# Performance work log

Measured on AMD Instinct MI355X. Metric: run time of the kernel, lower is better.

## Reference

```python
import jax, jax.numpy as jnp
import numpy as np

KDIM = 256
KNN = 32
VALUE_EXPAND = 4
EPS = 1e-5


def _ln_last(x, w):
    # LayerNorm over last axis with affine weight w (no bias)
    m = jnp.mean(x, axis=-1, keepdims=True)
    v = jnp.var(x, axis=-1, keepdims=True)
    return (x - m) * jax.lax.rsqrt(v + EPS) * w


def setup_inputs() -> dict:
    key = jax.random.key(0)
    ks = jax.random.split(key, 10)
    B, S, H = 2, 2048, 2048
    head, rank, mh = 2, 2, 2
    key_num = 1024
    value_num = 262144
    vvn = VALUE_EXPAND * value_num  # 1048576
    vdim = 256
    return {
        "hidden_state": jax.random.normal(ks[0], (B, S, H), jnp.float32),
        "wq": jax.random.normal(ks[1], (H, 2 * KDIM), jnp.float32) / np.sqrt(KDIM),
        "qnorm_w": jnp.full((KDIM,), 1.0 / KDIM ** 0.33, jnp.float32),
        "knorm_w": jnp.full((KDIM,), 1.0 / KDIM ** 0.33, jnp.float32),
        "keys": jax.random.normal(ks[2], (head, 2, key_num, KDIM, rank), jnp.float32) / np.sqrt(KDIM),
        "tucker_core": jax.random.uniform(ks[3], (mh, head, rank, rank), jnp.float32),
        "tucker_u": jax.random.normal(ks[4], (1, head, 1, rank), jnp.float32),
        "tucker_v": jax.random.normal(ks[5], (1, head, 1, rank), jnp.float32),
        "values": jax.random.normal(ks[6], (value_num, vdim), jnp.float32) * 0.02,
        "wv": jax.random.normal(ks[7], (VALUE_EXPAND * vdim, H), jnp.float32) / np.sqrt(VALUE_EXPAND * vdim),
        "shuffle_index": jax.random.permutation(ks[8], vvn).astype(jnp.int32),
    }


def reference(hidden_state, wq, qnorm_w, knorm_w, keys, tucker_core,
              tucker_u, tucker_v, values, wv, shuffle_index):
    B, S, H = hidden_state.shape
    bs = B * S
    head, _, key_num, kdim, rank = keys.shape
    value_num, vdim = values.shape

    # query projection + per-half layernorm
    q = (hidden_state.reshape(bs, H) @ wq).reshape(bs, 2, kdim)
    q = _ln_last(q, qnorm_w)
    q1, q2 = q[:, 0], q[:, 1]  # (bs, kdim)

    # keys layernorm over kdim (axis=-2)
    km = jnp.mean(keys, axis=-2, keepdims=True)
    kv = jnp.var(keys, axis=-2, keepdims=True)
    keysn = (keys - km) * jax.lax.rsqrt(kv + EPS) * knorm_w[:, None]

    # per-head, per-rank inner products (all heads share the single query; nhead_share_query=2)
    s1r = jnp.einsum("bd,hkdr->bhkr", q1, keysn[:, 0])  # (bs, head, key_num, rank)
    s2r = jnp.einsum("bd,hkdr->bhkr", q2, keysn[:, 1])

    # rank-1 tucker fused scores + topk along keys
    s1 = (s1r * tucker_u).sum(-1)  # (bs, head, key_num)
    s2 = (s2r * tucker_v).sum(-1)
    _, i1 = jax.lax.top_k(s1, KNN)  # (bs, head, knn)
    _, i2 = jax.lax.top_k(s2, KNN)

    g1 = jnp.take_along_axis(s1r, i1[..., None], axis=2)  # (bs, head, knn, rank)
    g2 = jnp.take_along_axis(s2r, i2[..., None], axis=2)

    # full tucker scores on the knn x knn candidate grid, summed over tucker heads
    all_scores = jnp.einsum("bhkr,mhrs,bhls->bhkl", g1, tucker_core, g2).reshape(bs, head, KNN * KNN)
    all_indices = (i1[..., :, None] * key_num + i2[..., None, :]).reshape(bs, head, KNN * KNN)

    best_scores, bi = jax.lax.top_k(all_scores, KNN)  # (bs, head, knn)
    best_indice = jnp.take_along_axis(all_indices, bi, axis=-1)

    # implicit value expansion: shuffled virtual index -> (expand slot, real value)
    shuffled = shuffle_index[best_indice]
    vidx = shuffled % value_num
    eidx = shuffled // value_num  # in [0, VALUE_EXPAND)
    vals = values[vidx]  # (bs, head, knn, vdim)
    w = jax.nn.softmax(best_scores, axis=-1)
    oh = jax.nn.one_hot(eidx, VALUE_EXPAND, dtype=vals.dtype)  # (bs, head, knn, E)
    agg = jnp.einsum("bhke,bhkv->bev", oh, w[..., None] * vals).reshape(bs, VALUE_EXPAND * vdim)
    out = agg @ wv  # (bs, H)
    return out.reshape(B, S, H)
```

## Files before the change

### kernel.cpp

```cpp
#include <hip/hip_runtime.h>
#include <float.h>
#include <math.h>


typedef __attribute__((ext_vector_type(8))) __bf16 bf16x8;
typedef __attribute__((ext_vector_type(4))) float f32x4;

__device__ __forceinline__ unsigned short f2bf(float x) {
  unsigned int u = __float_as_uint(x);
  return (unsigned short)((u + 0x7FFFu + ((u >> 16) & 1u)) >> 16);
}

__device__ __forceinline__ float wave_sum(float x) {
#pragma unroll
  for (int o = 32; o; o >>= 1) x += __shfl_xor(x, o, 64);
  return x;
}

__device__ __forceinline__ void gll16(const float* g, float* l) {
  __builtin_amdgcn_global_load_lds(
      (const __attribute__((address_space(1))) void*)g,
      (__attribute__((address_space(3))) void*)l, 16, 0, 0);
}

__device__ __forceinline__ unsigned int f2key(float f) {
  const unsigned int u = __float_as_uint(f);
  return u ^ (((unsigned int)((int)u >> 31)) | 0x80000000u);
}
__device__ __forceinline__ float key2f(unsigned int k) {
  return __uint_as_float((k & 0x80000000u) ? (k ^ 0x80000000u) : ~k);
}

__global__ void k_prep32(const float* __restrict__ keys, const float* __restrict__ knw,
                         const float* __restrict__ tu, const float* __restrict__ tv,
                         float* __restrict__ Bct, float* __restrict__ Bg) {
  const int bid = blockIdx.x;
  const int lane = threadIdx.x;
  const int k = bid & 1023, h = (bid >> 10) & 1, c = bid >> 11;
  const float* base = keys + (size_t)((h * 2 + c) * 1024 + k) * 512;
  float x0[4], x1[4];
  float s0 = 0.f, s1 = 0.f, sq0 = 0.f, sq1 = 0.f;
#pragma unroll
  for (int i = 0; i < 4; ++i) {
    const int d = lane + i * 64;
    const float2 p = *(const float2*)&base[d * 2];
    x0[i] = p.x; x1[i] = p.y;
    s0 += p.x; sq0 += p.x * p.x;
    s1 += p.y; sq1 += p.y * p.y;
  }
  s0 = wave_sum(s0); sq0 = wave_sum(sq0);
  s1 = wave_sum(s1); sq1 = wave_sum(sq1);
  const float m0 = s0 * (1.f / 256.f), m1 = s1 * (1.f / 256.f);
  const float rs0 = 1.f / sqrtf(sq0 * (1.f / 256.f) - m0 * m0 + 1e-5f);
  const float rs1 = 1.f / sqrtf(sq1 * (1.f / 256.f) - m1 * m1 + 1e-5f);
  const float* uv = c ? tv : tu;
  const float u0 = uv[h * 2 + 0], u1 = uv[h * 2 + 1];
  const int chk = c * 2048 + h * 1024 + k;
  float* bg = Bg + (size_t)chk * 512;
  float* bc = Bct + (size_t)chk * 256;
#pragma unroll
  for (int i = 0; i < 4; ++i) {
    const int d = lane + i * 64;
    const float w = knw[d];
    const float y0 = (x0[i] - m0) * rs0 * w;
    const float y1 = (x1[i] - m1) * rs1 * w;
    bg[d] = y0;
    bg[256 + d] = y1;
    bc[d] = y0 * u0 + y1 * u1;
  }
}

__global__ __launch_bounds__(256) void k_tr32(const float* __restrict__ src,
                                              float* __restrict__ dst, int R, int C) {
  __shared__ float t[64][65];
  const int br = blockIdx.x * 64, bc = blockIdx.y * 64;
  const int tid = threadIdx.x;
  for (int idx = tid; idx < 4096; idx += 256) {
    const int r = idx >> 6, c = idx & 63;
    t[r][c] = src[(size_t)(br + r) * C + bc + c];
  }
  __syncthreads();
  for (int idx = tid; idx < 4096; idx += 256) {
    const int cc = idx >> 6, rr = idx & 63;
    dst[(size_t)(bc + cc) * R + br + rr] = t[rr][cc];
  }
}

template <int SPLITK>
__global__ __launch_bounds__(256) void k_gemm32(
    const float* __restrict__ AT, int lda,
    const float* __restrict__ BT, int ldb, int bsk, int m_split,
    float* __restrict__ C, int M, int N, int K) {
  constexpr int BK = 16;
  __shared__ float As[2][BK][128];
  __shared__ float Bs[2][BK][128];
  const int tid = threadIdx.x;
  const int lane = tid & 63;
  const int w = tid >> 6;
  const int tx = tid & 15, ty = tid >> 4;
  const int bm = blockIdx.x * 128, bn = blockIdx.y * 128;
  const int bcol = bn + ((bm >= m_split) ? bsk : 0);
  const int Ks = K / SPLITK;
  const int kbeg = blockIdx.z * Ks;
  float* Cp = C + (size_t)blockIdx.z * M * N;
  const int l5 = lane >> 5, l31 = lane & 31;
  float acc[8][8] = {};

  auto stage = [&](int buf, int t) {
    const int k0 = t * BK;
#pragma unroll
    for (int i = 0; i < 2; ++i) {
      const int rr = w * 4 + i * 2;
      const size_t krow = (size_t)(kbeg + k0 + rr + l5);
      gll16(&AT[krow * lda + bm + l31 * 4], &As[buf][rr][0]);
      gll16(&BT[krow * ldb + bcol + l31 * 4], &Bs[buf][rr][0]);
    }
  };

  const int T = Ks / BK;
  stage(0, 0);
  __syncthreads();
  int cur = 0;
  for (int t = 0; t < T; ++t) {
    if (t + 1 < T) stage(cur ^ 1, t + 1);
#pragma unroll
    for (int kk = 0; kk < BK; ++kk) {
      float a[8], b[8];
      *(float4*)&a[0] = *(const float4*)&As[cur][kk][ty * 4];
      *(float4*)&a[4] = *(const float4*)&As[cur][kk][64 + ty * 4];
      *(float4*)&b[0] = *(const float4*)&Bs[cur][kk][tx * 4];
      *(float4*)&b[4] = *(const float4*)&Bs[cur][kk][64 + tx * 4];
#pragma unroll
      for (int i = 0; i < 8; ++i)
#pragma unroll
        for (int j = 0; j < 8; ++j) acc[i][j] += a[i] * b[j];
    }
    __syncthreads();
    cur ^= 1;
  }
#pragma unroll
  for (int ih = 0; ih < 2; ++ih)
#pragma unroll
    for (int i = 0; i < 4; ++i) {
      const size_t r = bm + ih * 64 + ty * 4 + i;
#pragma unroll
      for (int jh = 0; jh < 2; ++jh) {
        float4 v = {acc[ih * 4 + i][jh * 4 + 0], acc[ih * 4 + i][jh * 4 + 1],
                    acc[ih * 4 + i][jh * 4 + 2], acc[ih * 4 + i][jh * 4 + 3]};
        *(float4*)&Cp[r * N + bn + jh * 64 + tx * 4] = v;
      }
    }
}

__global__ void k_ln_q(const float* __restrict__ qpart, const float* __restrict__ qnw,
                       float* __restrict__ q12n) {
  const int bid = blockIdx.x;
  const int lane = threadIdx.x;
  const int b = bid >> 1, c = bid & 1;
  float x[4] = {};
#pragma unroll
  for (int s = 0; s < 4; ++s) {
    const float4 p = *(const float4*)&qpart[(size_t)s * 4096 * 512 + (size_t)b * 512 + c * 256 + lane * 4];
    x[0] += p.x; x[1] += p.y; x[2] += p.z; x[3] += p.w;
  }
  float sm = x[0] + x[1] + x[2] + x[3];
  float sq = x[0] * x[0] + x[1] * x[1] + x[2] * x[2] + x[3] * x[3];
  sm = wave_sum(sm);
  sq = wave_sum(sq);
  const float mean = sm * (1.f / 256.f);
  const float rs = 1.f / sqrtf(sq * (1.f / 256.f) - mean * mean + 1e-5f);
  const float4 w4 = *(const float4*)&qnw[lane * 4];
  float4 o;
  o.x = (x[0] - mean) * rs * w4.x;
  o.y = (x[1] - mean) * rs * w4.y;
  o.z = (x[2] - mean) * rs * w4.z;
  o.w = (x[3] - mean) * rs * w4.w;
  *(float4*)&q12n[(size_t)(c * 4096 + b) * 256 + lane * 4] = o;
}

__global__ void k_topk1(const float* __restrict__ s_r,
                        int* __restrict__ i1, int* __restrict__ i2) {
  const int bid = blockIdx.x;
  const int side = bid >> 13;
  const int bh = bid & 8191;
  const int b = bh >> 1, h = bh & 1;
  const int lane = threadIdx.x;
  const float* row = s_r + (size_t)(side * 4096 + b) * 2048 + h * 1024;
  unsigned int ku[16];
#pragma unroll
  for (int i = 0; i < 16; ++i) ku[i] = f2key(row[lane + (i << 6)]);
  unsigned int T = 0u;
  for (int bpos = 31; bpos >= 0; --bpos) {
    const unsigned int cand = T | (1u << bpos);
    int c = 0;
#pragma unroll
    for (int i = 0; i < 16; ++i) c += (ku[i] >= cand) ? 1 : 0;
#pragma unroll
    for (int o = 32; o; o >>= 1) c += __shfl_xor(c, o, 64);
    if (c >= 32) T = cand;
  }
  int cgt = 0, ceq = 0;
#pragma unroll
  for (int i = 0; i < 16; ++i) {
    cgt += (ku[i] > T) ? 1 : 0;
    ceq += (ku[i] == T) ? 1 : 0;
  }
  int pgt = cgt, peq = ceq;
#pragma unroll
  for (int o = 1; o < 64; o <<= 1) {
    const int t1 = __shfl_up(pgt, o, 64);
    const int t2 = __shfl_up(peq, o, 64);
    if (lane >= o) { pgt += t1; peq += t2; }
  }
  const int total_gt = __shfl(pgt, 63, 64);
  const int need_eq = 32 - total_gt;
  int sgt = pgt - cgt;
  int seq = peq - ceq;
  int* iout = (side ? i2 : i1) + bh * 32;
#pragma unroll
  for (int i = 0; i < 16; ++i) {
    const int idx = (i << 6) + lane;
    if (ku[i] > T) {
      iout[sgt++] = idx;
    } else if (ku[i] == T) {
      if (seq < need_eq) iout[total_gt + seq] = idx;
      ++seq;
    }
  }
}

__global__ __launch_bounds__(256) void k_gather(
    const float* __restrict__ q12n, const float* __restrict__ Bg,
    const int* __restrict__ i1, const int* __restrict__ i2,
    float* __restrict__ g1, float* __restrict__ g2) {
  __shared__ float qs[256];
  __shared__ int ssel[32];
  const int bid = blockIdx.x;
  const int side = bid >> 13;
  const int bh = bid & 8191;
  const int b = bh >> 1, h = bh & 1;
  const int tid = threadIdx.x;
  if (tid < 64) {
    *(float4*)&qs[tid * 4] =
        *(const float4*)&q12n[(size_t)(side * 4096 + b) * 256 + tid * 4];
  } else if (tid < 96) {
    ssel[tid - 64] = (side ? i2 : i1)[bh * 32 + (tid - 64)];
  }
  __syncthreads();
  const int j = tid >> 2;
  const int c4 = tid & 3;
  const int slot = j >> 1, r = j & 1;
  const int sel = ssel[slot];
  const float* krow =
      Bg + ((size_t)(side * 2048 + h * 1024 + sel) * 2 + r) * 256;
  float px = 0.f, py = 0.f, pz = 0.f, pw = 0.f;
#pragma unroll
  for (int i = 0; i < 16; ++i) {
    const int e = (i * 4 + c4) * 4;
    const float4 kv = *(const float4*)&krow[e];
    const float4 qv = *(const float4*)&qs[e];
    px += kv.x * qv.x;
    py += kv.y * qv.y;
    pz += kv.z * qv.z;
    pw += kv.w * qv.w;
  }
  float acc = (px + py) + (pz + pw);
  acc += __shfl_xor(acc, 1, 64);
  acc += __shfl_xor(acc, 2, 64);
  if (c4 == 0) (side ? g2 : g1)[(bh * 32 + slot) * 2 + r] = acc;
}

__global__ void k_stage2(const float* __restrict__ g1, const float* __restrict__ g2,
                         const int* __restrict__ i1, const int* __restrict__ i2,
                         const float* __restrict__ tucker_core,
                         const int* __restrict__ shuffle_index,
                         float* __restrict__ w_out, int* __restrict__ sh_out) {
  __shared__ float sg1x[32], sg1y[32], sg2x[32], sg2y[32];
  __shared__ int si1[32], si2[32];
  const int bh = blockIdx.x;
  const int h = bh & 1;
  const int lane = threadIdx.x;
  if (lane < 32) {
    const float2 p1 = *(const float2*)&g1[(bh * 32 + lane) * 2];
    const float2 p2 = *(const float2*)&g2[(bh * 32 + lane) * 2];
    sg1x[lane] = p1.x;
    sg1y[lane] = p1.y;
    sg2x[lane] = p2.x;
    sg2y[lane] = p2.y;
    si1[lane] = i1[bh * 32 + lane];
    si2[lane] = i2[bh * 32 + lane];
  }
  __syncthreads();
  const float c00 = tucker_core[h * 4 + 0] + tucker_core[8 + h * 4 + 0];
  const float c01 = tucker_core[h * 4 + 1] + tucker_core[8 + h * 4 + 1];
  const float c10 = tucker_core[h * 4 + 2] + tucker_core[8 + h * 4 + 2];
  const float c11 = tucker_core[h * 4 + 3] + tucker_core[8 + h * 4 + 3];
  float sv[16];
  unsigned int ku[16];
  float m = -FLT_MAX;
#pragma unroll
  for (int i = 0; i < 16; ++i) {
    const int p = lane + (i << 6);
    const int k = p >> 5, l = p & 31;
    const float a0 = sg1x[k] * c00 + sg1y[k] * c10;
    const float a1 = sg1x[k] * c01 + sg1y[k] * c11;
    sv[i] = a0 * sg2x[l] + a1 * sg2y[l];
    ku[i] = f2key(sv[i]);
    m = fmaxf(m, sv[i]);
  }
#pragma unroll
  for (int o = 32; o; o >>= 1) m = fmaxf(m, __shfl_xor(m, o, 64));
  unsigned int T = 0u;
  for (int bpos = 31; bpos >= 0; --bpos) {
    const unsigned int cand = T | (1u << bpos);
    int c = 0;
#pragma unroll
    for (int i = 0; i < 16; ++i) c += (ku[i] >= cand) ? 1 : 0;
#pragma unroll
    for (int o = 32; o; o >>= 1) c += __shfl_xor(c, o, 64);
    if (c >= 32) T = cand;
  }
  int cgt = 0, ceq = 0;
  float zp = 0.f;
#pragma unroll
  for (int i = 0; i < 16; ++i) {
    if (ku[i] > T) { ++cgt; zp += expf(sv[i] - m); }
    ceq += (ku[i] == T) ? 1 : 0;
  }
  int pgt = cgt, peq = ceq;
#pragma unroll
  for (int o = 1; o < 64; o <<= 1) {
    const int t1 = __shfl_up(pgt, o, 64);
    const int t2 = __shfl_up(peq, o, 64);
    if (lane >= o) { pgt += t1; peq += t2; }
  }
  const int total_gt = __shfl(pgt, 63, 64);
  const int need_eq = 32 - total_gt;
  const float eT = expf(key2f(T) - m);
  const float Z = wave_sum(zp) + (float)need_eq * eT;
  const float rZ = 1.f / Z;
  int sgt = pgt - cgt;
  int seq = peq - ceq;
  float* wp = w_out + bh * 32;
  int* shp = sh_out + bh * 32;
#pragma unroll
  for (int i = 0; i < 16; ++i) {
    int slot = -1;
    if (ku[i] > T) {
      slot = sgt++;
    } else if (ku[i] == T) {
      if (seq < need_eq) slot = total_gt + seq;
      ++seq;
    }
    if (slot >= 0) {
      const int p = lane + (i << 6);
      const int k = p >> 5, l = p & 31;
      const int ai = si1[k] * 1024 + si2[l];
      wp[slot] = expf(sv[i] - m) * rZ;
      shp[slot] = shuffle_index[ai];
    }
  }
}

__global__ __launch_bounds__(256) void k_agg(const float* __restrict__ w_out,
                                             const int* __restrict__ sh_out,
                                             const float* __restrict__ values,
                                             unsigned short* __restrict__ aggb) {
  __shared__ float acc[4][1024];
  const int b = blockIdx.x;
  const int tid = threadIdx.x;
  const int wave = tid >> 6, lane = tid & 63;
  for (int i = tid; i < 4096; i += 256) ((float*)acc)[i] = 0.f;
  __syncthreads();
  for (int j = wave; j < 64; j += 4) {
    const float wgt = w_out[b * 64 + j];
    const int sh = sh_out[b * 64 + j];
    const int vidx = sh & 0x3FFFF;
    const int e = sh >> 18;
    const float4 v = *(const float4*)&values[(size_t)vidx * 256 + lane * 4];
    float* dst = &acc[wave][e * 256 + lane * 4];
    dst[0] += wgt * v.x;
    dst[1] += wgt * v.y;
    dst[2] += wgt * v.z;
    dst[3] += wgt * v.w;
  }
  __syncthreads();
  for (int i = tid; i < 1024; i += 256)
    aggb[(size_t)b * 1024 + i] = f2bf(acc[0][i] + acc[1][i] + acc[2][i] + acc[3][i]);
}

__global__ __launch_bounds__(256) void k_tcvt(const float* __restrict__ src,
                                              unsigned short* __restrict__ dst,
                                              int R, int C) {
  __shared__ float tile[64][65];
  const int br = blockIdx.x * 64;
  const int bc = blockIdx.y * 64;
  const int tid = threadIdx.x;
  for (int idx = tid; idx < 4096; idx += 256) {
    const int r = idx >> 6, c = idx & 63;
    tile[r][c] = src[(size_t)(br + r) * C + bc + c];
  }
  __syncthreads();
  for (int idx = tid; idx < 4096; idx += 256) {
    const int cc = idx >> 6, rr = idx & 63;
    dst[(size_t)(bc + cc) * R + br + rr] = f2bf(tile[rr][cc]);
  }
}

template <int BM, int BN>
__global__ __launch_bounds__(256) void k_mfma(const unsigned short* __restrict__ A,
                                              const unsigned short* __restrict__ Bt,
                                              float* __restrict__ C,
                                              int M, int N, int K) {
  constexpr int FM = BM / 32;
  constexpr int FN = BN / 32;
  __shared__ float4 As[BM * 4];
  __shared__ float4 Bs[BN * 4];
  const int tid = threadIdx.x;
  const int lane = tid & 63;
  const int w = tid >> 6;
  const int wr = w >> 1, wc = w & 1;
  const int bm = blockIdx.x * BM, bn = blockIdx.y * BN;
  f32x4 acc[FM][FN];
#pragma unroll
  for (int i = 0; i < FM; ++i)
#pragma unroll
    for (int j = 0; j < FN; ++j) acc[i][j] = 0.f;

  for (int k0 = 0; k0 < K; k0 += 32) {
#pragma unroll
    for (int u = 0; u < BM * 4 / 256; ++u) {
      const int q = tid + u * 256;
      const int m = q >> 2, c = q & 3;
      As[(m >> 4) * 64 + c * 16 + (m & 15)] =
          *(const float4*)&A[(size_t)(bm + m) * K + k0 + c * 8];
    }
#pragma unroll
    for (int u = 0; u < BN * 4 / 256; ++u) {
      const int q = tid + u * 256;
      const int n = q >> 2, c = q & 3;
      Bs[(n >> 4) * 64 + c * 16 + (n & 15)] =
          *(const float4*)&Bt[(size_t)(bn + n) * K + k0 + c * 8];
    }
    __syncthreads();
    bf16x8 af[FM], bfr[FN];
#pragma unroll
    for (int i = 0; i < FM; ++i) af[i] = *(const bf16x8*)&As[(wr * FM + i) * 64 + lane];
#pragma unroll
    for (int j = 0; j < FN; ++j) bfr[j] = *(const bf16x8*)&Bs[(wc * FN + j) * 64 + lane];
#pragma unroll
    for (int i = 0; i < FM; ++i)
#pragma unroll
      for (int j = 0; j < FN; ++j)
        acc[i][j] = __builtin_amdgcn_mfma_f32_16x16x32_bf16(af[i], bfr[j], acc[i][j], 0, 0, 0);
    __syncthreads();
  }
#pragma unroll
  for (int i = 0; i < FM; ++i) {
    const int r0 = bm + (wr * FM + i) * 16 + (lane >> 4) * 4;
#pragma unroll
    for (int j = 0; j < FN; ++j) {
      const int cc = bn + (wc * FN + j) * 16 + (lane & 15);
#pragma unroll
      for (int v = 0; v < 4; ++v) C[(size_t)(r0 + v) * N + cc] = acc[i][j][v];
    }
  }
}

extern "C" void kernel_launch(void* const* d_in, const int* in_sizes, int n_in,
                              void* d_out, int out_size, void* d_ws, size_t ws_size,
                              hipStream_t stream) {
  const float* hidden = (const float*)d_in[0];
  const float* wq     = (const float*)d_in[1];
  const float* qnw    = (const float*)d_in[2];
  const float* knw    = (const float*)d_in[3];
  const float* keys   = (const float*)d_in[4];
  const float* tcore  = (const float*)d_in[5];
  const float* tu     = (const float*)d_in[6];
  const float* tv     = (const float*)d_in[7];
  const float* values = (const float*)d_in[8];
  const float* wvm    = (const float*)d_in[9];
  const int*   shuf   = (const int*)d_in[10];
  float* out = (float*)d_out;

  char* ws = (char*)d_ws;
  size_t off = 0;
  auto alloc = [&](size_t bytes) -> void* {
    void* p = ws + off;
    off += (bytes + 255) & ~(size_t)255;
    return p;
  };
  float* Bct   = (float*)alloc((size_t)4096 * 256 * 4);
  float* BctT  = (float*)alloc((size_t)256 * 4096 * 4);
  float* Bg    = (float*)alloc((size_t)4096 * 512 * 4);
  float* q12n  = (float*)alloc((size_t)8192 * 256 * 4);
  float* q12nT = (float*)alloc((size_t)256 * 8192 * 4);
  unsigned short* wvT  = (unsigned short*)alloc((size_t)2048 * 1024 * 2);
  unsigned short* aggb = (unsigned short*)alloc((size_t)4096 * 1024 * 2);
  int*   i1  = (int*)  alloc((size_t)8192 * 32 * 4);
  int*   i2  = (int*)  alloc((size_t)8192 * 32 * 4);
  float* g1  = (float*)alloc((size_t)8192 * 64 * 4);
  float* g2  = (float*)alloc((size_t)8192 * 64 * 4);
  float* wgt = (float*)alloc((size_t)8192 * 32 * 4);
  int*   sho = (int*)  alloc((size_t)8192 * 32 * 4);
  float* hiddenT = (float*)alloc((size_t)2048 * 4096 * 4);
  float* big = (float*)alloc((size_t)8192 * 2048 * 4);
  float* qpart = big;
  float* s_r   = big;
  (void)ws_size; (void)in_sizes; (void)n_in; (void)out_size;

  k_prep32<<<4096, 64, 0, stream>>>(keys, knw, tu, tv, Bct, Bg);
  k_tcvt<<<dim3(16, 32), 256, 0, stream>>>(wvm, wvT, 1024, 2048);
  k_tr32<<<dim3(64, 4), 256, 0, stream>>>(Bct, BctT, 4096, 256);
  k_tr32<<<dim3(64, 32), 256, 0, stream>>>(hidden, hiddenT, 4096, 2048);
  k_gemm32<4><<<dim3(32, 4, 4), 256, 0, stream>>>(
      hiddenT, 4096, wq, 512, 0, 1 << 30, qpart, 4096, 512, 2048);
  k_ln_q<<<8192, 64, 0, stream>>>(qpart, qnw, q12n);
  k_tr32<<<dim3(128, 4), 256, 0, stream>>>(q12n, q12nT, 8192, 256);
  k_gemm32<1><<<dim3(64, 16, 1), 256, 0, stream>>>(
      q12nT, 8192, BctT, 4096, 2048, 4096, s_r, 8192, 2048, 256);
  k_topk1<<<16384, 64, 0, stream>>>(s_r, i1, i2);
  k_gather<<<16384, 256, 0, stream>>>(q12n, Bg, i1, i2, g1, g2);
  k_stage2<<<8192, 64, 0, stream>>>(g1, g2, i1, i2, tcore, shuf, wgt, sho);
  k_agg<<<4096, 256, 0, stream>>>(wgt, sho, values, aggb);
  k_mfma<128, 128><<<dim3(32, 16), 256, 0, stream>>>(aggb, wvT, out, 4096, 2048, 1024);
}
```

Before: 465.6 us.

## Compute coarse key scores with bf16 MFMA and rescore 48 candidates in fp32

The first-stage score GEMM now runs through the bf16 MFMA kernel using bf16 copies of the normalized queries and keys, which removes two transposes and the fp32 GEMM. To make up for bf16 rounding, the first top-k keeps 48 candidates per row. A new selection kernel recomputes their exact fp32 scores and picks the final 32 with a ballot-based radix select. Ballot/popcount replaces shuffle reductions in the top-k loops. The risk is that a true top-32 key falls outside the bf16 top-48, plus extra gather work for 48 rows.

```diff
diff --git a/kernel.cpp b/kernel.cpp
--- a/kernel.cpp
+++ b/kernel.cpp
@@ -33,7 +33,7 @@
 
 __global__ void k_prep32(const float* __restrict__ keys, const float* __restrict__ knw,
                          const float* __restrict__ tu, const float* __restrict__ tv,
-                         float* __restrict__ Bct, float* __restrict__ Bg) {
+                         unsigned short* __restrict__ Bctbf, float* __restrict__ Bg) {
   const int bid = blockIdx.x;
   const int lane = threadIdx.x;
   const int k = bid & 1023, h = (bid >> 10) & 1, c = bid >> 11;
@@ -57,7 +57,7 @@
   const float u0 = uv[h * 2 + 0], u1 = uv[h * 2 + 1];
   const int chk = c * 2048 + h * 1024 + k;
   float* bg = Bg + (size_t)chk * 512;
-  float* bc = Bct + (size_t)chk * 256;
+  unsigned short* bc = Bctbf + (size_t)chk * 256;
 #pragma unroll
   for (int i = 0; i < 4; ++i) {
     const int d = lane + i * 64;
@@ -66,7 +66,7 @@
     const float y1 = (x1[i] - m1) * rs1 * w;
     bg[d] = y0;
     bg[256 + d] = y1;
-    bc[d] = y0 * u0 + y1 * u1;
+    bc[d] = f2bf(y0 * u0 + y1 * u1);
   }
 }
 
@@ -153,7 +153,7 @@
 }
 
 __global__ void k_ln_q(const float* __restrict__ qpart, const float* __restrict__ qnw,
-                       float* __restrict__ q12n) {
+                       float* __restrict__ q12n, unsigned short* __restrict__ q12bf) {
   const int bid = blockIdx.x;
   const int lane = threadIdx.x;
   const int b = bid >> 1, c = bid & 1;
@@ -175,11 +175,15 @@
   o.y = (x[1] - mean) * rs * w4.y;
   o.z = (x[2] - mean) * rs * w4.z;
   o.w = (x[3] - mean) * rs * w4.w;
-  *(float4*)&q12n[(size_t)(c * 4096 + b) * 256 + lane * 4] = o;
+  const size_t base = (size_t)(c * 4096 + b) * 256 + lane * 4;
+  *(float4*)&q12n[base] = o;
+  ushort4 ob;
+  ob.x = f2bf(o.x); ob.y = f2bf(o.y); ob.z = f2bf(o.z); ob.w = f2bf(o.w);
+  *(ushort4*)&q12bf[base] = ob;
 }
 
 __global__ void k_topk1(const float* __restrict__ s_r,
-                        int* __restrict__ i1, int* __restrict__ i2) {
+                        int* __restrict__ i1c, int* __restrict__ i2c) {
   const int bid = blockIdx.x;
   const int side = bid >> 13;
   const int bh = bid & 8191;
@@ -194,10 +198,8 @@
     const unsigned int cand = T | (1u << bpos);
     int c = 0;
 #pragma unroll
-    for (int i = 0; i < 16; ++i) c += (ku[i] >= cand) ? 1 : 0;
-#pragma unroll
-    for (int o = 32; o; o >>= 1) c += __shfl_xor(c, o, 64);
-    if (c >= 32) T = cand;
+    for (int i = 0; i < 16; ++i) c += (int)__popcll(__ballot(ku[i] >= cand));
+    if (c >= 48) T = cand;
   }
   int cgt = 0, ceq = 0;
 #pragma unroll
@@ -213,10 +215,10 @@
     if (lane >= o) { pgt += t1; peq += t2; }
   }
   const int total_gt = __shfl(pgt, 63, 64);
-  const int need_eq = 32 - total_gt;
+  const int need_eq = 48 - total_gt;
   int sgt = pgt - cgt;
   int seq = peq - ceq;
-  int* iout = (side ? i2 : i1) + bh * 32;
+  int* iout = (side ? i2c : i1c) + bh * 48;
 #pragma unroll
   for (int i = 0; i < 16; ++i) {
     const int idx = (i << 6) + lane;
@@ -229,12 +231,15 @@
   }
 }
 
-__global__ __launch_bounds__(256) void k_gather(
+__global__ __launch_bounds__(256) void k_sel(
     const float* __restrict__ q12n, const float* __restrict__ Bg,
-    const int* __restrict__ i1, const int* __restrict__ i2,
+    const int* __restrict__ i1c, const int* __restrict__ i2c,
+    const float* __restrict__ tu, const float* __restrict__ tv,
+    int* __restrict__ i1, int* __restrict__ i2,
     float* __restrict__ g1, float* __restrict__ g2) {
   __shared__ float qs[256];
-  __shared__ int ssel[32];
+  __shared__ int ssel[48];
+  __shared__ float sc[48], sd0[48], sd1[48];
   const int bid = blockIdx.x;
   const int side = bid >> 13;
   const int bh = bid & 8191;
@@ -243,31 +248,71 @@
   if (tid < 64) {
     *(float4*)&qs[tid * 4] =
         *(const float4*)&q12n[(size_t)(side * 4096 + b) * 256 + tid * 4];
-  } else if (tid < 96) {
-    ssel[tid - 64] = (side ? i2 : i1)[bh * 32 + (tid - 64)];
-  }
-  __syncthreads();
-  const int j = tid >> 2;
-  const int c4 = tid & 3;
-  const int slot = j >> 1, r = j & 1;
-  const int sel = ssel[slot];
-  const float* krow =
-      Bg + ((size_t)(side * 2048 + h * 1024 + sel) * 2 + r) * 256;
-  float px = 0.f, py = 0.f, pz = 0.f, pw = 0.f;
-#pragma unroll
-  for (int i = 0; i < 16; ++i) {
-    const int e = (i * 4 + c4) * 4;
-    const float4 kv = *(const float4*)&krow[e];
-    const float4 qv = *(const float4*)&qs[e];
-    px += kv.x * qv.x;
-    py += kv.y * qv.y;
-    pz += kv.z * qv.z;
-    pw += kv.w * qv.w;
-  }
-  float acc = (px + py) + (pz + pw);
-  acc += __shfl_xor(acc, 1, 64);
-  acc += __shfl_xor(acc, 2, 64);
-  if (c4 == 0) (side ? g2 : g1)[(bh * 32 + slot) * 2 + r] = acc;
+  } else if (tid < 112) {
+    ssel[tid - 64] = (side ? i2c : i1c)[bh * 48 + (tid - 64)];
+  }
+  __syncthreads();
+  const int g = tid >> 2, c4 = tid & 3;
+  if (g < 48) {
+    const int sel = ssel[g];
+    const float* kbase = Bg + (size_t)((side * 2048 + h * 1024 + sel) * 2) * 256;
+    float d0 = 0.f, d1 = 0.f;
+#pragma unroll
+    for (int r = 0; r < 2; ++r) {
+      const float* krow = kbase + r * 256;
+      float px = 0.f, py = 0.f, pz = 0.f, pw = 0.f;
+#pragma unroll
+      for (int i = 0; i < 16; ++i) {
+        const int e = (i * 4 + c4) * 4;
+        const float4 kv = *(const float4*)&krow[e];
+        const float4 qv = *(const float4*)&qs[e];
+        px += kv.x * qv.x;
+        py += kv.y * qv.y;
+        pz += kv.z * qv.z;
+        pw += kv.w * qv.w;
+      }
+      float a = (px + py) + (pz + pw);
+      a += __shfl_xor(a, 1, 64);
+      a += __shfl_xor(a, 2, 64);
+      if (r == 0) d0 = a; else d1 = a;
+    }
+    if (c4 == 0) {
+      const float* uv = side ? tv : tu;
+      sd0[g] = d0;
+      sd1[g] = d1;
+      sc[g] = d0 * uv[h * 2 + 0] + d1 * uv[h * 2 + 1];
+    }
+  }
+  __syncthreads();
+  if (tid < 64) {
+    const int lane = tid;
+    const unsigned int kv = (lane < 48) ? f2key(sc[lane]) : 0u;
+    unsigned int T = 0u;
+    for (int bpos = 31; bpos >= 0; --bpos) {
+      const unsigned int cand = T | (1u << bpos);
+      const int c = (int)__popcll(__ballot(kv >= cand));
+      if (c >= 32) T = cand;
+    }
+    const unsigned long long mgt = __ballot(kv > T);
+    const unsigned long long meq = __ballot((kv == T) && (lane < 48));
+    const unsigned long long below = ((unsigned long long)1 << lane) - 1;
+    const int total_gt = (int)__popcll(mgt);
+    const int need = 32 - total_gt;
+    int slot = -1;
+    if (kv > T) {
+      slot = (int)__popcll(mgt & below);
+    } else if (kv == T && lane < 48) {
+      const int r = (int)__popcll(meq & below);
+      if (r < need) slot = total_gt + r;
+    }
+    if (slot >= 0) {
+      int* iout = (side ? i2 : i1) + bh * 32;
+      float* gout = (side ? g2 : g1) + (size_t)bh * 64;
+      iout[slot] = ssel[lane];
+      gout[slot * 2 + 0] = sd0[lane];
+      gout[slot * 2 + 1] = sd1[lane];
+    }
+  }
 }
 
 __global__ void k_stage2(const float* __restrict__ g1, const float* __restrict__ g2,
@@ -315,9 +360,7 @@
     const unsigned int cand = T | (1u << bpos);
     int c = 0;
 #pragma unroll
-    for (int i = 0; i < 16; ++i) c += (ku[i] >= cand) ? 1 : 0;
-#pragma unroll
-    for (int o = 32; o; o >>= 1) c += __shfl_xor(c, o, 64);
+    for (int i = 0; i < 16; ++i) c += (int)__popcll(__ballot(ku[i] >= cand));
     if (c >= 32) T = cand;
   }
   int cgt = 0, ceq = 0;
@@ -411,7 +454,8 @@
 __global__ __launch_bounds__(256) void k_mfma(const unsigned short* __restrict__ A,
                                               const unsigned short* __restrict__ Bt,
                                               float* __restrict__ C,
-                                              int M, int N, int K) {
+                                              int M, int N, int K,
+                                              int bsk, int m_split) {
   constexpr int FM = BM / 32;
   constexpr int FN = BN / 32;
   __shared__ float4 As[BM * 4];
@@ -421,6 +465,7 @@
   const int w = tid >> 6;
   const int wr = w >> 1, wc = w & 1;
   const int bm = blockIdx.x * BM, bn = blockIdx.y * BN;
+  const int bcol = bn + ((bm >= m_split) ? bsk : 0);
   f32x4 acc[FM][FN];
 #pragma unroll
   for (int i = 0; i < FM; ++i)
@@ -440,7 +485,7 @@
       const int q = tid + u * 256;
       const int n = q >> 2, c = q & 3;
       Bs[(n >> 4) * 64 + c * 16 + (n & 15)] =
-          *(const float4*)&Bt[(size_t)(bn + n) * K + k0 + c * 8];
+          *(const float4*)&Bt[(size_t)(bcol + n) * K + k0 + c * 8];
     }
     __syncthreads();
     bf16x8 af[FM], bfr[FN];
@@ -490,13 +535,14 @@
     off += (bytes + 255) & ~(size_t)255;
     return p;
   };
-  float* Bct   = (float*)alloc((size_t)4096 * 256 * 4);
-  float* BctT  = (float*)alloc((size_t)256 * 4096 * 4);
+  unsigned short* Bctbf = (unsigned short*)alloc((size_t)4096 * 256 * 2);
   float* Bg    = (float*)alloc((size_t)4096 * 512 * 4);
   float* q12n  = (float*)alloc((size_t)8192 * 256 * 4);
-  float* q12nT = (float*)alloc((size_t)256 * 8192 * 4);
+  unsigned short* q12bf = (unsigned short*)alloc((size_t)8192 * 256 * 2);
   unsigned short* wvT  = (unsigned short*)alloc((size_t)2048 * 1024 * 2);
   unsigned short* aggb = (unsigned short*)alloc((size_t)4096 * 1024 * 2);
+  int*   i1c = (int*)  alloc((size_t)8192 * 48 * 4);
+  int*   i2c = (int*)  alloc((size_t)8192 * 48 * 4);
   int*   i1  = (int*)  alloc((size_t)8192 * 32 * 4);
   int*   i2  = (int*)  alloc((size_t)8192 * 32 * 4);
   float* g1  = (float*)alloc((size_t)8192 * 64 * 4);
@@ -509,19 +555,18 @@
   float* s_r   = big;
   (void)ws_size; (void)in_sizes; (void)n_in; (void)out_size;
 
-  k_prep32<<<4096, 64, 0, stream>>>(keys, knw, tu, tv, Bct, Bg);
+  k_prep32<<<4096, 64, 0, stream>>>(keys, knw, tu, tv, Bctbf, Bg);
   k_tcvt<<<dim3(16, 32), 256, 0, stream>>>(wvm, wvT, 1024, 2048);
-  k_tr32<<<dim3(64, 4), 256, 0, stream>>>(Bct, BctT, 4096, 256);
   k_tr32<<<dim3(64, 32), 256, 0, stream>>>(hidden, hiddenT, 4096, 2048);
   k_gemm32<4><<<dim3(32, 4, 4), 256, 0, stream>>>(
       hiddenT, 4096, wq, 512, 0, 1 << 30, qpart, 4096, 512, 2048);
-  k_ln_q<<<8192, 64, 0, stream>>>(qpart, qnw, q12n);
-  k_tr32<<<dim3(128, 4), 256, 0, stream>>>(q12n, q12nT, 8192, 256);
-  k_gemm32<1><<<dim3(64, 16, 1), 256, 0, stream>>>(
-      q12nT, 8192, BctT, 4096, 2048, 4096, s_r, 8192, 2048, 256);
-  k_topk1<<<16384, 64, 0, stream>>>(s_r, i1, i2);
-  k_gather<<<16384, 256, 0, stream>>>(q12n, Bg, i1, i2, g1, g2);
+  k_ln_q<<<8192, 64, 0, stream>>>(qpart, qnw, q12n, q12bf);
+  k_mfma<128, 128><<<dim3(64, 16), 256, 0, stream>>>(
+      q12bf, Bctbf, s_r, 8192, 2048, 256, 2048, 4096);
+  k_topk1<<<16384, 64, 0, stream>>>(s_r, i1c, i2c);
+  k_sel<<<16384, 256, 0, stream>>>(q12n, Bg, i1c, i2c, tu, tv, i1, i2, g1, g2);
   k_stage2<<<8192, 64, 0, stream>>>(g1, g2, i1, i2, tcore, shuf, wgt, sho);
   k_agg<<<4096, 256, 0, stream>>>(wgt, sho, values, aggb);
-  k_mfma<128, 128><<<dim3(32, 16), 256, 0, stream>>>(aggb, wvT, out, 4096, 2048, 1024);
-}
+  k_mfma<128, 128><<<dim3(32, 16), 256, 0, stream>>>(
+      aggb, wvT, out, 4096, 2048, 1024, 0, 1 << 30);
+}
```

Result: faster. 393.1 us (-15.6%).
